# Kernel optimization log

Measured on AMD Instinct MI355X. Metric: run time of the kernel, lower is better.

Reference implementation:

```python
import jax, jax.numpy as jnp
import numpy as np

NEG_SLOPE = 0.2

def setup_inputs() -> dict:
    key = jax.random.key(0)
    k1, k2, k3, k4 = jax.random.split(key, 4)
    B, n, d_in, d_out = 8, 2048, 128, 128
    x = jax.random.normal(k1, (B, n, d_in), dtype=jnp.float32)
    adj = jax.random.uniform(k2, (B, n, n), dtype=jnp.float32)
    # glorot init for W: std = sqrt(2/(fan_in+fan_out))
    W = jax.random.normal(k3, (d_in, d_out), dtype=jnp.float32) * np.sqrt(2.0 / (d_in + d_out))
    a = jax.random.normal(k4, (2 * d_out,), dtype=jnp.float32) * np.sqrt(2.0 / (2 * d_out + 1))
    return {"x": x, "adj": adj, "W": W, "a": a}

def reference(x, adj, W, a):
    d_out = W.shape[1]
    h = jnp.einsum('bni,io->bno', x, W)               # [B,n,d_out]
    x_weighted = jnp.einsum('bnm,bmo->bno', adj, h)   # adj @ Wx
    # additive attention: a @ concat(h_i, h_j) == h_i@a_src + h_j@a_dst
    a_src, a_dst = a[:d_out], a[d_out:]
    s_i = h @ a_src                                   # [B,n]
    s_j = h @ a_dst                                   # [B,n]
    e = jax.nn.leaky_relu(s_i[:, :, None] + s_j[:, None, :], NEG_SLOPE)  # [B,n,n]
    alpha = jax.nn.softmax(e, axis=2)
    out = jnp.einsum('bnm,bmo->bno', alpha, h) + x_weighted
    return jax.nn.leaky_relu(out, NEG_SLOPE)
```

## Files before the change

### kernel.cpp

```cpp
#include <hip/hip_runtime.h>
#include <hip/hip_bf16.h>

#define NEG 0.2f
#define LOG2E 1.4426950408889634f

typedef __attribute__((ext_vector_type(8))) short bf16x8;
typedef __attribute__((ext_vector_type(4))) float f32x4;
typedef __attribute__((ext_vector_type(16))) float f32x16;
typedef __attribute__((ext_vector_type(4))) int int4v;

__device__ __forceinline__ float lrelu(float t){ return fmaxf(t, NEG * t); }
__device__ __forceinline__ float fast_exp2(float x){
  float r; asm("v_exp_f32 %0, %1" : "=v"(r) : "v"(x)); return r;
}
__device__ __forceinline__ unsigned short f2bf(float f){
  union { float f; unsigned int u; } v; v.f = f;
  unsigned int r = v.u + 0x7FFFu + ((v.u >> 16) & 1u);
  return (unsigned short)(r >> 16);
}

__global__ __launch_bounds__(256) void k0_wt(const float* __restrict__ W,
                                             unsigned short* __restrict__ Wt){
  __shared__ __align__(16) unsigned short wl[128*136];
  const int t = threadIdx.x;
  {
    const int k = t >> 1, oh = (t & 1) * 64;
#pragma unroll 8
    for (int e = 0; e < 64; ++e)
      wl[(oh + e)*136 + k] = f2bf(W[k*128 + oh + e]);
  }
  __syncthreads();
  {
    const int o = t >> 1, ks = (t & 1) * 64;
#pragma unroll
    for (int g = 0; g < 8; ++g){
      int4v v = *(const int4v*)(wl + o*136 + ks + g*8);
      *(int4v*)(Wt + o*128 + ks + g*8) = v;
    }
  }
}

__global__ __launch_bounds__(256) void k1_fused(const float* __restrict__ x,
                                                const unsigned short* __restrict__ Wt,
                                                const float* __restrict__ a,
                                                unsigned short* __restrict__ ht,
                                                float* __restrict__ ssrcL,
                                                float* __restrict__ sdstL){
  __shared__ __align__(16) unsigned short wtl[128*136];
  __shared__ __align__(16) unsigned short xl[32*136];
  __shared__ __align__(16) unsigned short tlw[128*34];
  __shared__ float sred[2][4][2][16];
  const int t = threadIdx.x;
  const int bx = blockIdx.x;
  const int b  = bx >> 6;
  const int jt = bx & 63;
  const long rowbase = (long)bx * 32;
  {
    const int o = t >> 1, seg = (t & 1) * 64;
    const int4v* src = (const int4v*)(Wt + o*128 + seg);
    int4v* dst = (int4v*)(wtl + o*136 + seg);
#pragma unroll
    for (int g = 0; g < 8; ++g) dst[g] = src[g];
  }
  {
    const int i = t >> 3, ks = (t & 7) * 16;
    const f32x4* src = (const f32x4*)(x + (rowbase + i)*128 + ks);
    unsigned int q[8];
#pragma unroll
    for (int g = 0; g < 4; ++g){
      f32x4 v = src[g];
      q[g*2]   = (unsigned)f2bf(v[0]) | ((unsigned)f2bf(v[1]) << 16);
      q[g*2+1] = (unsigned)f2bf(v[2]) | ((unsigned)f2bf(v[3]) << 16);
    }
    int4v* dst = (int4v*)(xl + i*136 + ks);
    dst[0] = *(int4v*)&q[0];
    dst[1] = *(int4v*)&q[4];
  }
  __syncthreads();
  const int w = t >> 6, lane = t & 63, lr = lane & 15, hi = lane >> 4;
  f32x4 zro = {0.f, 0.f, 0.f, 0.f};
  f32x4 acc00 = zro, acc01 = zro, acc10 = zro, acc11 = zro;
#pragma unroll
  for (int ks = 0; ks < 4; ++ks){
    const bf16x8 a0 = *(const bf16x8*)(wtl + (w*32      + lr)*136 + ks*32 + hi*8);
    const bf16x8 a1 = *(const bf16x8*)(wtl + (w*32 + 16 + lr)*136 + ks*32 + hi*8);
    const bf16x8 b0 = *(const bf16x8*)(xl + (     lr)*136 + ks*32 + hi*8);
    const bf16x8 b1 = *(const bf16x8*)(xl + (16 + lr)*136 + ks*32 + hi*8);
    acc00 = __builtin_amdgcn_mfma_f32_16x16x32_bf16(a0, b0, acc00, 0, 0, 0);
    acc01 = __builtin_amdgcn_mfma_f32_16x16x32_bf16(a0, b1, acc01, 0, 0, 0);
    acc10 = __builtin_amdgcn_mfma_f32_16x16x32_bf16(a1, b0, acc10, 0, 0, 0);
    acc11 = __builtin_amdgcn_mfma_f32_16x16x32_bf16(a1, b1, acc11, 0, 0, 0);
  }
  {
    const f32x4 as0 = *(const f32x4*)(a +       w*32      + hi*4);
    const f32x4 as1 = *(const f32x4*)(a +       w*32 + 16 + hi*4);
    const f32x4 ad0 = *(const f32x4*)(a + 128 + w*32      + hi*4);
    const f32x4 ad1 = *(const f32x4*)(a + 128 + w*32 + 16 + hi*4);
    float ps0, ps1, pd0, pd1;
    {
      f32x4 u = acc00*as0 + acc10*as1;  ps0 = u[0]+u[1]+u[2]+u[3];
      f32x4 v = acc01*as0 + acc11*as1;  ps1 = v[0]+v[1]+v[2]+v[3];
      f32x4 p = acc00*ad0 + acc10*ad1;  pd0 = p[0]+p[1]+p[2]+p[3];
      f32x4 r = acc01*ad0 + acc11*ad1;  pd1 = r[0]+r[1]+r[2]+r[3];
    }
#pragma unroll
    for (int off = 16; off <= 32; off <<= 1){
      ps0 += __shfl_xor(ps0, off); ps1 += __shfl_xor(ps1, off);
      pd0 += __shfl_xor(pd0, off); pd1 += __shfl_xor(pd1, off);
    }
    if (hi == 0){
      sred[0][w][0][lr] = ps0; sred[0][w][1][lr] = ps1;
      sred[1][w][0][lr] = pd0; sred[1][w][1][lr] = pd1;
    }
  }
#pragma unroll
  for (int q = 0; q < 4; ++q){
    tlw[(w*32      + hi*4 + q)*34      + lr] = f2bf(acc00[q]);
    tlw[(w*32      + hi*4 + q)*34 + 16 + lr] = f2bf(acc01[q]);
    tlw[(w*32 + 16 + hi*4 + q)*34      + lr] = f2bf(acc10[q]);
    tlw[(w*32 + 16 + hi*4 + q)*34 + 16 + lr] = f2bf(acc11[q]);
  }
  __syncthreads();
  {
    const int o = t >> 1, jseg = (t & 1) * 16;
    const unsigned int* src = (const unsigned int*)(tlw + o*34 + jseg);
    unsigned int p[8];
#pragma unroll
    for (int g = 0; g < 8; ++g) p[g] = src[g];
    unsigned short* dst = ht + (long)b*262144 + (long)o*2048 + jt*32 + jseg;
    ((int4v*)dst)[0] = *(int4v*)&p[0];
    ((int4v*)dst)[1] = *(int4v*)&p[4];
  }
  if (t < 64){
    const int sel = t >> 5, jl = t & 31;
    const int ig = jl >> 4, l2 = jl & 15;
    const float s = sred[sel][0][ig][l2] + sred[sel][1][ig][l2]
                  + sred[sel][2][ig][l2] + sred[sel][3][ig][l2];
    if (sel == 0) ssrcL[rowbase + jl] = s * LOG2E;
    else          sdstL[rowbase + jl] = s * LOG2E;
  }
}

__global__ __launch_bounds__(256) void k2_ml(const float* __restrict__ ssrcL,
                                             const float* __restrict__ sdstL,
                                             float* __restrict__ carr){
  const int lane = threadIdx.x & 63;
  const long row = (long)blockIdx.x * 4 + (threadIdx.x >> 6);
  const int b = (int)(row >> 11);
  const float siL = ssrcL[row];
  const float* sd = sdstL + (long)b*2048;
  float mx = -3.4e38f;
#pragma unroll
  for (int k = 0; k < 8; ++k){
    f32x4 v = *(const f32x4*)(sd + lane*4 + k*256);
    mx = fmaxf(mx, fmaxf(fmaxf(v[0], v[1]), fmaxf(v[2], v[3])));
  }
#pragma unroll
  for (int off = 1; off <= 32; off <<= 1) mx = fmaxf(mx, __shfl_xor(mx, off));
  const float mL = lrelu(siL + mx);
  float sum = 0.f;
#pragma unroll
  for (int k = 0; k < 8; ++k){
    f32x4 v = *(const f32x4*)(sd + lane*4 + k*256);
#pragma unroll
    for (int e = 0; e < 4; ++e) sum += fast_exp2(lrelu(siL + v[e]) - mL);
  }
#pragma unroll
  for (int off = 1; off <= 32; off <<= 1) sum += __shfl_xor(sum, off);
  if (lane == 0) carr[row] = mL + __log2f(sum);
}

__global__ __launch_bounds__(128) void k3_main(const float* __restrict__ adj,
                                               const unsigned short* __restrict__ ht,
                                               const float* __restrict__ ssrcL,
                                               const float* __restrict__ sdstL,
                                               const float* __restrict__ carr,
                                               float* __restrict__ out){
  __shared__ __align__(16) char smem[65536];
  unsigned short (*tl)[2][128][64] = (unsigned short (*)[2][128][64])smem;
  float* red = (float*)smem;
  const int t   = threadIdx.x;
  const int bxr = blockIdx.x;
  const int bx  = ((bxr & 7) << 6) | (bxr >> 3);
  const int b   = bx >> 6;
  const int i0  = (bx & 63) * 32;
  const int w   = t >> 6, lane = t & 63;
  const int r32 = lane & 31, ks = lane >> 5;
  const long rowg = (long)b*2048 + i0 + r32;
  const float siL = ssrcL[rowg];
  const float Ci  = carr[rowg];
  const float* adjrow = adj + rowg*2048 + w*1024;
  const float* sdb    = sdstL + (long)b*2048 + w*1024;
  const unsigned short* sgbase = ht + (long)b*262144 + w*1024
                               + ((lane & 7) ^ ((lane >> 3) & 7)) * 8
                               + (long)(lane >> 3) * 2048;

#define K3_STAGE(BB, JB) do{                                                     \
    _Pragma("unroll")                                                            \
    for (int ii = 0; ii < 16; ++ii){                                             \
      __builtin_amdgcn_global_load_lds(                                          \
        (const __attribute__((address_space(1))) void*)(sgbase + (JB) + ii*16384),\
        (__attribute__((address_space(3))) void*)&tl[BB][w][ii*8][0], 16, 0, 0); \
    }                                                                            \
    __builtin_amdgcn_sched_barrier(0);                                           \
  }while(0)

#define K3_LOADSET(SL, JB) do{                                                   \
    _Pragma("unroll")                                                            \
    for (int g = 0; g < 4; ++g){                                                 \
      av[SL][g*2]   = *(const f32x4*)(adjrow + (JB) + g*16 + ks*8);              \
      av[SL][g*2+1] = *(const f32x4*)(adjrow + (JB) + g*16 + ks*8 + 4);          \
      dv[SL][g*2]   = *(const f32x4*)(sdb    + (JB) + g*16 + ks*8);              \
      dv[SL][g*2+1] = *(const f32x4*)(sdb    + (JB) + g*16 + ks*8 + 4);          \
    }                                                                            \
  }while(0)

  f32x4 av[2][8], dv[2][8];
  f32x16 acc[4];
#pragma unroll
  for (int f = 0; f < 4; ++f)
#pragma unroll
    for (int e = 0; e < 16; ++e) acc[f][e] = 0.f;

  K3_STAGE(0, 0);
  K3_LOADSET(0, 0);
  K3_LOADSET(1, 64);
  asm volatile("s_waitcnt vmcnt(32)" ::: "memory");
  __builtin_amdgcn_sched_barrier(0);

#pragma unroll
  for (int i = 0; i < 16; ++i){
    const int cur = i & 1;
    if (i < 15) K3_STAGE(cur ^ 1, (i + 1) * 64);
    bf16x8 af[4];
#pragma unroll
    for (int g = 0; g < 4; ++g){
      float wv[8];
#pragma unroll
      for (int e = 0; e < 4; ++e){
        wv[e]     = av[cur][g*2][e]   + fast_exp2(lrelu(siL + dv[cur][g*2][e])   - Ci);
        wv[4 + e] = av[cur][g*2+1][e] + fast_exp2(lrelu(siL + dv[cur][g*2+1][e]) - Ci);
      }
      const unsigned int p01 = __builtin_amdgcn_perm(__float_as_uint(wv[1]), __float_as_uint(wv[0]), 0x07060302u);
      const unsigned int p23 = __builtin_amdgcn_perm(__float_as_uint(wv[3]), __float_as_uint(wv[2]), 0x07060302u);
      const unsigned int p45 = __builtin_amdgcn_perm(__float_as_uint(wv[5]), __float_as_uint(wv[4]), 0x07060302u);
      const unsigned int p67 = __builtin_amdgcn_perm(__float_as_uint(wv[7]), __float_as_uint(wv[6]), 0x07060302u);
      int4v ai = {(int)p01, (int)p23, (int)p45, (int)p67};
      af[g] = *(bf16x8*)&ai;
    }
    if (i < 14) K3_LOADSET(cur, (i + 2) * 64);
#pragma unroll
    for (int g = 0; g < 4; ++g){
      const int cph = ((g*2 + ks) ^ (lane & 7)) * 8;
#pragma unroll
      for (int f = 0; f < 4; ++f){
        const bf16x8 bf = *(const bf16x8*)&tl[cur][w][f*32 + r32][cph];
        acc[f] = __builtin_amdgcn_mfma_f32_32x32x16_bf16(af[g], bf, acc[f], 0, 0, 0);
      }
    }
    if (i < 14)      asm volatile("s_waitcnt vmcnt(16)" ::: "memory");
    else if (i == 14) asm volatile("s_waitcnt vmcnt(0)"  ::: "memory");
    __builtin_amdgcn_sched_barrier(0);
  }
#undef K3_STAGE
#undef K3_LOADSET

  __syncthreads();
  if (w == 1){
#pragma unroll
    for (int f = 0; f < 4; ++f)
#pragma unroll
      for (int rg = 0; rg < 16; ++rg){
        const int rr = (rg & 3) + 8*(rg >> 2) + 4*ks;
        red[rr*128 + f*32 + r32] = acc[f][rg];
      }
  }
  __syncthreads();
  if (w == 0){
#pragma unroll
    for (int f = 0; f < 4; ++f)
#pragma unroll
      for (int rg = 0; rg < 16; ++rg){
        const int rr = (rg & 3) + 8*(rg >> 2) + 4*ks;
        const float v = acc[f][rg] + red[rr*128 + f*32 + r32];
        out[((long)b*2048 + i0 + rr)*128 + f*32 + r32] = lrelu(v);
      }
  }
}

extern "C" void kernel_launch(void* const* d_in, const int* in_sizes, int n_in,
                              void* d_out, int out_size, void* d_ws, size_t ws_size,
                              hipStream_t stream){
  const float* x   = (const float*)d_in[0];
  const float* adj = (const float*)d_in[1];
  const float* W   = (const float*)d_in[2];
  const float* a   = (const float*)d_in[3];
  float* out = (float*)d_out;
  char* ws = (char*)d_ws;

  unsigned short* ht    = (unsigned short*)(ws);
  float*          ssrcL = (float*)(ws + 4194304);
  float*          sdstL = (float*)(ws + 4259840);
  float*          carr  = (float*)(ws + 4325376);
  unsigned short* Wt    = (unsigned short*)(ws + 4390912);

  k0_wt   <<<1,    256, 0, stream>>>(W, Wt);
  k1_fused<<<512,  256, 0, stream>>>(x, Wt, a, ht, ssrcL, sdstL);
  k2_ml   <<<4096, 256, 0, stream>>>(ssrcL, sdstL, carr);
  k3_main <<<512,  128, 0, stream>>>(adj, ht, ssrcL, sdstL, carr, out);
}
```

Measured before the change: 64.55 us.

## Split k3 work across output columns with shared weight tile instead of K-split

The main kernel moves from two waves that split the j (K) dimension and reduce partial sums through LDS to four waves that each own 32 output columns across the full K range. The attention weights are computed once per 64-column step, written to a swizzled LDS tile, and shared by all waves after a block barrier. This removes the final cross-wave reduction and the fourfold per-wave accumulator. In exchange it adds a barrier every step and an extra LDS round trip for the weights, and launches 256 threads with an occupancy hint.

```diff
diff --git a/kernel.cpp b/kernel.cpp
--- a/kernel.cpp
+++ b/kernel.cpp
@@ -170,121 +170,103 @@
   if (lane == 0) carr[row] = mL + __log2f(sum);
 }
 
-__global__ __launch_bounds__(128) void k3_main(const float* __restrict__ adj,
-                                               const unsigned short* __restrict__ ht,
-                                               const float* __restrict__ ssrcL,
-                                               const float* __restrict__ sdstL,
-                                               const float* __restrict__ carr,
-                                               float* __restrict__ out){
-  __shared__ __align__(16) char smem[65536];
-  unsigned short (*tl)[2][128][64] = (unsigned short (*)[2][128][64])smem;
-  float* red = (float*)smem;
-  const int t   = threadIdx.x;
-  const int bxr = blockIdx.x;
-  const int bx  = ((bxr & 7) << 6) | (bxr >> 3);
-  const int b   = bx >> 6;
-  const int i0  = (bx & 63) * 32;
-  const int w   = t >> 6, lane = t & 63;
-  const int r32 = lane & 31, ks = lane >> 5;
+__global__ __launch_bounds__(256, 2) void k3_main(const float* __restrict__ adj,
+                                                  const unsigned short* __restrict__ ht,
+                                                  const float* __restrict__ ssrcL,
+                                                  const float* __restrict__ sdstL,
+                                                  const float* __restrict__ carr,
+                                                  float* __restrict__ out){
+  __shared__ __align__(16) unsigned short httile[2][128][64];
+  __shared__ __align__(16) unsigned short wtile[2][32][64];
+  const int t    = threadIdx.x;
+  const int bxr  = blockIdx.x;
+  const int bx   = ((bxr & 7) << 6) | (bxr >> 3);
+  const int b    = bx >> 6;
+  const int i0   = (bx & 63) * 32;
+  const int w    = t >> 6, lane = t & 63;
+  const int r32  = lane & 31, hl = lane >> 5;
+  const int r7   = r32 & 7;
+  const int wchunk = (w*2 + hl) ^ r7;
   const long rowg = (long)b*2048 + i0 + r32;
   const float siL = ssrcL[rowg];
   const float Ci  = carr[rowg];
-  const float* adjrow = adj + rowg*2048 + w*1024;
-  const float* sdb    = sdstL + (long)b*2048 + w*1024;
-  const unsigned short* sgbase = ht + (long)b*262144 + w*1024
-                               + ((lane & 7) ^ ((lane >> 3) & 7)) * 8
-                               + (long)(lane >> 3) * 2048;
-
-#define K3_STAGE(BB, JB) do{                                                     \
+  const float* adjL = adj + rowg*2048 + w*16 + hl*8;
+  const float* sdbL = sdstL + (long)b*2048 + w*16 + hl*8;
+  const unsigned short* sgbase = ht + (long)b*262144
+                               + (long)(w*32 + (lane >> 3))*2048
+                               + ((lane & 7) ^ (lane >> 3)) * 8;
+
+  f32x16 acc;
+#pragma unroll
+  for (int e = 0; e < 16; ++e) acc[e] = 0.f;
+  f32x4 aA0, aA1, dA0, dA1, aB0, aB1, dB0, dB1;
+
+#pragma unroll
+  for (int it = 0; it < 4; ++it)
+    __builtin_amdgcn_global_load_lds(
+      (const __attribute__((address_space(1))) void*)(sgbase + it*16384),
+      (__attribute__((address_space(3))) void*)&httile[0][w*32 + it*8][0], 16, 0, 0);
+  aA0 = *(const f32x4*)(adjL);      aA1 = *(const f32x4*)(adjL + 4);
+  dA0 = *(const f32x4*)(sdbL);      dA1 = *(const f32x4*)(sdbL + 4);
+  aB0 = *(const f32x4*)(adjL + 64); aB1 = *(const f32x4*)(adjL + 68);
+  dB0 = *(const f32x4*)(sdbL + 64); dB1 = *(const f32x4*)(sdbL + 68);
+
+#define K3_STEP(JB, BUF, DO_STAGE, DO_REFILL, VMSTR, AV0, AV1, DV0, DV1) do{     \
+    if (DO_STAGE){                                                               \
+      _Pragma("unroll")                                                          \
+      for (int it = 0; it < 4; ++it)                                             \
+        __builtin_amdgcn_global_load_lds(                                        \
+          (const __attribute__((address_space(1))) void*)(sgbase + (JB) + 64 + it*16384), \
+          (__attribute__((address_space(3))) void*)&httile[(BUF)^1][w*32 + it*8][0], 16, 0, 0); \
+    }                                                                            \
+    {  float wv[8];                                                              \
+       _Pragma("unroll")                                                         \
+       for (int e = 0; e < 4; ++e){                                              \
+         wv[e]   = AV0[e] + fast_exp2(lrelu(siL + DV0[e]) - Ci);                 \
+         wv[4+e] = AV1[e] + fast_exp2(lrelu(siL + DV1[e]) - Ci);                 \
+       }                                                                         \
+       const unsigned p01 = __builtin_amdgcn_perm(__float_as_uint(wv[1]), __float_as_uint(wv[0]), 0x07060302u); \
+       const unsigned p23 = __builtin_amdgcn_perm(__float_as_uint(wv[3]), __float_as_uint(wv[2]), 0x07060302u); \
+       const unsigned p45 = __builtin_amdgcn_perm(__float_as_uint(wv[5]), __float_as_uint(wv[4]), 0x07060302u); \
+       const unsigned p67 = __builtin_amdgcn_perm(__float_as_uint(wv[7]), __float_as_uint(wv[6]), 0x07060302u); \
+       int4v ai = {(int)p01, (int)p23, (int)p45, (int)p67};                      \
+       *(int4v*)&wtile[BUF][r32][wchunk*8] = ai;                                 \
+    }                                                                            \
+    if (DO_REFILL){                                                              \
+      AV0 = *(const f32x4*)(adjL + (JB) + 128);                                  \
+      AV1 = *(const f32x4*)(adjL + (JB) + 132);                                  \
+      DV0 = *(const f32x4*)(sdbL + (JB) + 128);                                  \
+      DV1 = *(const f32x4*)(sdbL + (JB) + 132);                                  \
+    }                                                                            \
+    asm volatile("s_waitcnt vmcnt(" VMSTR ") lgkmcnt(0)" ::: "memory");          \
+    __builtin_amdgcn_sched_barrier(0);                                           \
+    __builtin_amdgcn_s_barrier();                                                \
+    __builtin_amdgcn_sched_barrier(0);                                           \
+    __builtin_amdgcn_s_setprio(1);                                               \
     _Pragma("unroll")                                                            \
-    for (int ii = 0; ii < 16; ++ii){                                             \
-      __builtin_amdgcn_global_load_lds(                                          \
-        (const __attribute__((address_space(1))) void*)(sgbase + (JB) + ii*16384),\
-        (__attribute__((address_space(3))) void*)&tl[BB][w][ii*8][0], 16, 0, 0); \
-    }                                                                            \
+    for (int g = 0; g < 4; ++g){                                                 \
+      const int pos = ((2*g + hl) ^ r7) * 8;                                     \
+      const bf16x8 afr = *(const bf16x8*)&wtile[BUF][r32][pos];                  \
+      const bf16x8 bfr = *(const bf16x8*)&httile[BUF][w*32 + r32][pos];          \
+      acc = __builtin_amdgcn_mfma_f32_32x32x16_bf16(afr, bfr, acc, 0, 0, 0);     \
+    }                                                                            \
+    __builtin_amdgcn_s_setprio(0);                                               \
     __builtin_amdgcn_sched_barrier(0);                                           \
   }while(0)
 
-#define K3_LOADSET(SL, JB) do{                                                   \
-    _Pragma("unroll")                                                            \
-    for (int g = 0; g < 4; ++g){                                                 \
-      av[SL][g*2]   = *(const f32x4*)(adjrow + (JB) + g*16 + ks*8);              \
-      av[SL][g*2+1] = *(const f32x4*)(adjrow + (JB) + g*16 + ks*8 + 4);          \
-      dv[SL][g*2]   = *(const f32x4*)(sdb    + (JB) + g*16 + ks*8);              \
-      dv[SL][g*2+1] = *(const f32x4*)(sdb    + (JB) + g*16 + ks*8 + 4);          \
-    }                                                                            \
-  }while(0)
-
-  f32x4 av[2][8], dv[2][8];
-  f32x16 acc[4];
-#pragma unroll
-  for (int f = 0; f < 4; ++f)
-#pragma unroll
-    for (int e = 0; e < 16; ++e) acc[f][e] = 0.f;
-
-  K3_STAGE(0, 0);
-  K3_LOADSET(0, 0);
-  K3_LOADSET(1, 64);
-  asm volatile("s_waitcnt vmcnt(32)" ::: "memory");
-  __builtin_amdgcn_sched_barrier(0);
-
-#pragma unroll
-  for (int i = 0; i < 16; ++i){
-    const int cur = i & 1;
-    if (i < 15) K3_STAGE(cur ^ 1, (i + 1) * 64);
-    bf16x8 af[4];
-#pragma unroll
-    for (int g = 0; g < 4; ++g){
-      float wv[8];
-#pragma unroll
-      for (int e = 0; e < 4; ++e){
-        wv[e]     = av[cur][g*2][e]   + fast_exp2(lrelu(siL + dv[cur][g*2][e])   - Ci);
-        wv[4 + e] = av[cur][g*2+1][e] + fast_exp2(lrelu(siL + dv[cur][g*2+1][e]) - Ci);
-      }
-      const unsigned int p01 = __builtin_amdgcn_perm(__float_as_uint(wv[1]), __float_as_uint(wv[0]), 0x07060302u);
-      const unsigned int p23 = __builtin_amdgcn_perm(__float_as_uint(wv[3]), __float_as_uint(wv[2]), 0x07060302u);
-      const unsigned int p45 = __builtin_amdgcn_perm(__float_as_uint(wv[5]), __float_as_uint(wv[4]), 0x07060302u);
-      const unsigned int p67 = __builtin_amdgcn_perm(__float_as_uint(wv[7]), __float_as_uint(wv[6]), 0x07060302u);
-      int4v ai = {(int)p01, (int)p23, (int)p45, (int)p67};
-      af[g] = *(bf16x8*)&ai;
-    }
-    if (i < 14) K3_LOADSET(cur, (i + 2) * 64);
-#pragma unroll
-    for (int g = 0; g < 4; ++g){
-      const int cph = ((g*2 + ks) ^ (lane & 7)) * 8;
-#pragma unroll
-      for (int f = 0; f < 4; ++f){
-        const bf16x8 bf = *(const bf16x8*)&tl[cur][w][f*32 + r32][cph];
-        acc[f] = __builtin_amdgcn_mfma_f32_32x32x16_bf16(af[g], bf, acc[f], 0, 0, 0);
-      }
-    }
-    if (i < 14)      asm volatile("s_waitcnt vmcnt(16)" ::: "memory");
-    else if (i == 14) asm volatile("s_waitcnt vmcnt(0)"  ::: "memory");
-    __builtin_amdgcn_sched_barrier(0);
-  }
-#undef K3_STAGE
-#undef K3_LOADSET
-
-  __syncthreads();
-  if (w == 1){
-#pragma unroll
-    for (int f = 0; f < 4; ++f)
-#pragma unroll
-      for (int rg = 0; rg < 16; ++rg){
-        const int rr = (rg & 3) + 8*(rg >> 2) + 4*ks;
-        red[rr*128 + f*32 + r32] = acc[f][rg];
-      }
-  }
-  __syncthreads();
-  if (w == 0){
-#pragma unroll
-    for (int f = 0; f < 4; ++f)
-#pragma unroll
-      for (int rg = 0; rg < 16; ++rg){
-        const int rr = (rg & 3) + 8*(rg >> 2) + 4*ks;
-        const float v = acc[f][rg] + red[rr*128 + f*32 + r32];
-        out[((long)b*2048 + i0 + rr)*128 + f*32 + r32] = lrelu(v);
-      }
+  for (int kt = 0; kt < 30; kt += 2){
+    const int jb0 = kt * 64;
+    K3_STEP(jb0,      0, 1, 1, "8", aA0, aA1, dA0, dA1);
+    K3_STEP(jb0 + 64, 1, 1, 1, "8", aB0, aB1, dB0, dB1);
+  }
+  K3_STEP(1920, 0, 1, 0, "8", aA0, aA1, dA0, dA1);
+  K3_STEP(1984, 1, 0, 0, "0", aB0, aB1, dB0, dB1);
+#undef K3_STEP
+
+#pragma unroll
+  for (int rg = 0; rg < 16; ++rg){
+    const int rr = (rg & 3) + 8*(rg >> 2) + 4*hl;
+    out[((long)b*2048 + i0 + rr)*128 + w*32 + r32] = lrelu(acc[rg]);
   }
 }
 
@@ -307,5 +289,5 @@
   k0_wt   <<<1,    256, 0, stream>>>(W, Wt);
   k1_fused<<<512,  256, 0, stream>>>(x, Wt, a, ht, ssrcL, sdstL);
   k2_ml   <<<4096, 256, 0, stream>>>(ssrcL, sdstL, carr);
-  k3_main <<<512,  128, 0, stream>>>(adj, ht, ssrcL, sdstL, carr, out);
-}
+  k3_main <<<512,  256, 0, stream>>>(adj, ht, ssrcL, sdstL, carr, out);
+}
```

After: 52.66 us. 1.23x faster.
